# Optimization experiments

Measured on AMD Instinct MI355X. Metric: run time of the kernel, lower is better.

Reference implementation:

```python
import jax, jax.numpy as jnp
import numpy as np

D_MODEL = 1024
NUM_HEADS = 16
HEAD_DIM = D_MODEL // NUM_HEADS
THETA = 10000.0


def _init_linear(key, d_out, d_in):
    sigma = np.sqrt(2.0 / (d_in + d_out))
    w = jax.random.truncated_normal(key, -3.0, 3.0, (d_out, d_in), dtype=jnp.float32)
    return w * sigma


def setup_inputs() -> dict:
    key = jax.random.key(0)
    kh, kq, kk, kv, ko = jax.random.split(key, 5)
    h = jax.random.normal(kh, (2, 2048, D_MODEL), dtype=jnp.float32)
    return {
        "h": h,
        "wq": _init_linear(kq, D_MODEL, D_MODEL),
        "wk": _init_linear(kk, D_MODEL, D_MODEL),
        "wv": _init_linear(kv, D_MODEL, D_MODEL),
        "wo": _init_linear(ko, D_MODEL, D_MODEL),
    }


def _rope(x, pos):
    # x: [B, H, T, dh]; rotate interleaved pairs (..., 2k, 2k+1)
    dh = x.shape[-1]
    freq = THETA ** (-jnp.arange(0, dh // 2, dtype=jnp.float32) / (dh // 2))
    ang = pos[:, None] * freq[None, :]            # [T, dh/2]
    cos, sin = jnp.cos(ang), jnp.sin(ang)
    xr = x.reshape(*x.shape[:-1], dh // 2, 2)
    x0, x1 = xr[..., 0], xr[..., 1]
    out = jnp.stack((cos * x0 - sin * x1, sin * x0 + cos * x1), axis=-1)
    return out.reshape(x.shape)


def reference(h, wq, wk, wv, wo):
    B, T, D = h.shape
    Hn, dh = NUM_HEADS, HEAD_DIM

    def split_heads(x):  # [B,T,D] -> [B,H,T,dh]
        return x.reshape(B, T, Hn, dh).transpose(0, 2, 1, 3)

    Q = split_heads(h @ wq.T)
    K = split_heads(h @ wk.T)
    V = split_heads(h @ wv.T)

    pos = jnp.arange(T, dtype=jnp.float32)
    Q = _rope(Q, pos)
    K = _rope(K, pos)

    scores = jnp.einsum('bhqd,bhkd->bhqk', Q, K) / jnp.sqrt(jnp.float32(dh))
    mask = jnp.tril(jnp.ones((T, T), dtype=bool))
    scores = jnp.where(mask, scores, -jnp.inf)
    attn = jax.nn.softmax(scores, axis=-1)
    out = jnp.einsum('bhqk,bhkd->bhqd', attn, V)   # [B,H,T,dh]
    out = out.transpose(0, 2, 1, 3).reshape(B, T, D)
    return out @ wo.T
```

## Files before the change

kernel.cpp:

```cpp
#include <hip/hip_runtime.h>
#include <math.h>

typedef __bf16 bf16_t;
typedef __bf16 v8bf __attribute__((ext_vector_type(8)));
typedef __bf16 v4bf __attribute__((ext_vector_type(4)));
typedef float  v4f  __attribute__((ext_vector_type(4)));

#define AS1 __attribute__((address_space(1)))
#define AS3 __attribute__((address_space(3)))

static __device__ __forceinline__ void load_lds16(const bf16_t* g, bf16_t* l) {
    __builtin_amdgcn_global_load_lds((AS1 void*)const_cast<bf16_t*>(g),
                                     (AS3 void*)l, 16, 0, 0);
}

__global__ __launch_bounds__(256) void cvt_fp32_bf16(
    const float* __restrict__ h,  const float* __restrict__ wq,
    const float* __restrict__ wk, const float* __restrict__ wv,
    const float* __restrict__ wo,
    bf16_t* __restrict__ hb,  bf16_t* __restrict__ wqb,
    bf16_t* __restrict__ wkb, bf16_t* __restrict__ wvb,
    bf16_t* __restrict__ wob)
{
    const size_t HM = (size_t)4 << 20;
    const size_t i8 = ((size_t)blockIdx.x * 256 + threadIdx.x) * 8;
    const float* src; bf16_t* dst; size_t off;
    if (i8 < HM) { src = h; dst = hb; off = i8; }
    else {
        const size_t r = (i8 - HM) >> 20;
        off = (i8 - HM) & (((size_t)1 << 20) - 1);
        src = (r == 0) ? wq  : (r == 1) ? wk  : (r == 2) ? wv  : wo;
        dst = (r == 0) ? wqb : (r == 1) ? wkb : (r == 2) ? wvb : wob;
    }
    const float4 a = *(const float4*)(src + off);
    const float4 b = *(const float4*)(src + off + 4);
    v8bf o;
    o[0]=(bf16_t)a.x; o[1]=(bf16_t)a.y; o[2]=(bf16_t)a.z; o[3]=(bf16_t)a.w;
    o[4]=(bf16_t)b.x; o[5]=(bf16_t)b.y; o[6]=(bf16_t)b.z; o[7]=(bf16_t)b.w;
    *(v8bf*)(dst + off) = o;
}

static __device__ __forceinline__ void fast_sincos(float ang, float* sn, float* cs) {
    float rv = ang * 0.15915494309189535f;
    rv -= floorf(rv);
    const float a = rv * 6.283185307179586f;
    *sn = __sinf(a);
    *cs = __cosf(a);
}

__global__ __launch_bounds__(256) void qkv_gemm_rope(
    const bf16_t* __restrict__ A,
    const bf16_t* __restrict__ wq,
    const bf16_t* __restrict__ wk,
    const bf16_t* __restrict__ wv,
    bf16_t* __restrict__ qo, bf16_t* __restrict__ ko, bf16_t* __restrict__ vo)
{
    __shared__ __align__(16) bf16_t smem[17408];
    bf16_t* As = smem;
    bf16_t* Bs = smem + 4096;

    const int tid = threadIdx.x;
    const int n0  = blockIdx.x * 128;
    const int m0  = blockIdx.y * 128;
    const int sel = n0 >> 10;
    const bf16_t* W = (sel == 0) ? wq : (sel == 1) ? wk : wv;
    const int wr0 = n0 & 1023;

    const int wave = tid >> 6;
    const int lane = tid & 63;
    const int l16  = lane & 15;
    const int quad = lane >> 4;
    const int wrow = (wave >> 1) * 64;
    const int wcol = (wave & 1) * 64;

    v4f acc[4][4];
    #pragma unroll
    for (int i = 0; i < 4; ++i)
        #pragma unroll
        for (int j = 0; j < 4; ++j) acc[i][j] = (v4f)(0.0f);

    for (int kt = 0; kt < 32; ++kt) {
        const int k0 = kt * 32;
        #pragma unroll
        for (int rep = 0; rep < 2; ++rep) {
            const int c   = rep * 256 + tid;
            const int row = c >> 2;
            const int col = (c & 3) * 8;
            load_lds16(A + (size_t)(m0 + row) * 1024 + k0 + col, &As[c * 8]);
            load_lds16(W + (size_t)(wr0 + row) * 1024 + k0 + col, &Bs[c * 8]);
        }
        __syncthreads();

        v8bf af[4], bfb[4];
        #pragma unroll
        for (int i = 0; i < 4; ++i) {
            af[i]  = *(const v8bf*)&As[(wrow + i * 16 + l16) * 32 + quad * 8];
            bfb[i] = *(const v8bf*)&Bs[(wcol + i * 16 + l16) * 32 + quad * 8];
        }
        #pragma unroll
        for (int i = 0; i < 4; ++i)
            #pragma unroll
            for (int j = 0; j < 4; ++j)
                acc[i][j] = __builtin_amdgcn_mfma_f32_16x16x32_bf16(
                    af[i], bfb[j], acc[i][j], 0, 0, 0);
        __syncthreads();
    }

    bf16_t* Ls = smem + wave * 4352;
    const int bq     = (m0 + wrow) >> 11;
    const int hd     = ((n0 + wcol) >> 6) & 15;
    const int t_base = (m0 + wrow) & 2047;

    if (sel < 2) {
        bf16_t* OUT = (sel == 0) ? qo : ko;
        #pragma unroll
        for (int i = 0; i < 4; ++i) {
            #pragma unroll
            for (int j = 0; j < 4; ++j) {
                #pragma unroll
                for (int r = 0; r < 4; ++r) {
                    const int mrow = i * 16 + quad * 4 + r;
                    const int dcol = j * 16 + l16;
                    float v = acc[i][j][r];
                    const float vp = __shfl_xor(v, 1);
                    const int t  = t_base + mrow;
                    const int kk = dcol >> 1;
                    const float freq = exp2f((float)kk * -0.4152410118609203f);
                    float sn, cs;
                    fast_sincos((float)t * freq, &sn, &cs);
                    v = ((dcol & 1) == 0) ? (cs * v - sn * vp) : (sn * vp + cs * v);
                    Ls[mrow * 68 + dcol] = (bf16_t)v;
                }
            }
        }
        #pragma unroll
        for (int s = 0; s < 8; ++s) {
            const int row = s * 8 + (lane >> 3);
            const int off = (lane & 7) * 8;
            const v8bf vv = *(const v8bf*)&Ls[row * 68 + off];
            *(v8bf*)(OUT + (((size_t)(bq * 16 + hd) * 2048) + t_base + row) * 64 + off) = vv;
        }
    } else {
        #pragma unroll
        for (int i = 0; i < 4; ++i)
            #pragma unroll
            for (int j = 0; j < 4; ++j) {
                v4bf p;
                #pragma unroll
                for (int r = 0; r < 4; ++r) p[r] = (bf16_t)acc[i][j][r];
                *(v4bf*)&Ls[(j * 16 + l16) * 68 + i * 16 + quad * 4] = p;
            }
        #pragma unroll
        for (int s = 0; s < 8; ++s) {
            const int drow = s * 8 + (lane >> 3);
            const int off  = (lane & 7) * 8;
            const v8bf vv = *(const v8bf*)&Ls[drow * 68 + off];
            *(v8bf*)(vo + (((size_t)(bq * 16 + hd) * 64) + drow) * 2048 + t_base + off) = vv;
        }
    }
}

__global__ __launch_bounds__(256) void attn_mfma(
    const bf16_t* __restrict__ qg,
    const bf16_t* __restrict__ kg,
    const bf16_t* __restrict__ vtg,
    bf16_t* __restrict__ og)
{
    __shared__ __align__(16) bf16_t Ks[64 * 72];
    __shared__ __align__(16) bf16_t Vs[64 * 72];
    __shared__ __align__(16) bf16_t Ps[4][16 * 72];

    const int tid  = threadIdx.x;
    const int wave = tid >> 6;
    const int lane = tid & 63;
    const int l16  = lane & 15;
    const int quad = lane >> 4;

    const int i    = blockIdx.x;
    const int pair = (i >> 3) & 15;
    const int bh   = (i & 7) * 4 + (i >> 7);
    const int b = bh >> 4, hh = bh & 15;

    const bf16_t* Kb = kg  + (size_t)bh * 2048 * 64;
    const bf16_t* Vb = vtg + (size_t)bh * 64 * 2048;

    #pragma unroll
    for (int pass = 0; pass < 2; ++pass) {
        const int qt   = pass ? pair : (31 - pair);
        const int qglb = qt * 64 + wave * 16 + l16;

        const bf16_t* qrow = qg + ((size_t)bh * 2048 + qglb) * 64;
        v8bf qf[2];
        qf[0] = *(const v8bf*)(qrow + quad * 8);
        qf[1] = *(const v8bf*)(qrow + 32 + quad * 8);
        #pragma unroll
        for (int e = 0; e < 8; ++e) {
            qf[0][e] = (bf16_t)((float)qf[0][e] * 0.125f);
            qf[1][e] = (bf16_t)((float)qf[1][e] * 0.125f);
        }

        float m_r = -1e30f, l_r = 0.0f;
        v4f o_acc[4];
        #pragma unroll
        for (int d = 0; d < 4; ++d) o_acc[d] = (v4f)(0.0f);

        v8bf kreg[2], vreg[2];
        #pragma unroll
        for (int rep = 0; rep < 2; ++rep) {
            const int c = rep * 256 + tid;
            const int row = c >> 3, col = (c & 7) * 8;
            kreg[rep] = *(const v8bf*)(Kb + (size_t)row * 64 + col);
            vreg[rep] = *(const v8bf*)(Vb + (size_t)row * 2048 + col);
        }

        for (int kt = 0; kt <= qt; ++kt) {
            __syncthreads();
            #pragma unroll
            for (int rep = 0; rep < 2; ++rep) {
                const int c = rep * 256 + tid;
                const int row = c >> 3, col = (c & 7) * 8;
                *(v8bf*)&Ks[row * 72 + col] = kreg[rep];
                *(v8bf*)&Vs[row * 72 + col] = vreg[rep];
            }
            __syncthreads();

            if (kt < qt) {
                #pragma unroll
                for (int rep = 0; rep < 2; ++rep) {
                    const int c = rep * 256 + tid;
                    const int row = c >> 3, col = (c & 7) * 8;
                    kreg[rep] = *(const v8bf*)(Kb + ((size_t)(kt + 1) * 64 + row) * 64 + col);
                    vreg[rep] = *(const v8bf*)(Vb + (size_t)row * 2048 + (kt + 1) * 64 + col);
                }
            }

            v4f s_acc[4];
            #pragma unroll
            for (int kblk = 0; kblk < 4; ++kblk) s_acc[kblk] = (v4f)(0.0f);
            #pragma unroll
            for (int kblk = 0; kblk < 4; ++kblk) {
                const v8bf kf0 = *(const v8bf*)&Ks[(kblk * 16 + l16) * 72 + quad * 8];
                const v8bf kf1 = *(const v8bf*)&Ks[(kblk * 16 + l16) * 72 + 32 + quad * 8];
                s_acc[kblk] = __builtin_amdgcn_mfma_f32_16x16x32_bf16(
                    kf0, qf[0], s_acc[kblk], 0, 0, 0);
                s_acc[kblk] = __builtin_amdgcn_mfma_f32_16x16x32_bf16(
                    kf1, qf[1], s_acc[kblk], 0, 0, 0);
            }

            if (kt == qt) {
                #pragma unroll
                for (int kblk = 0; kblk < 4; ++kblk)
                    #pragma unroll
                    for (int r = 0; r < 4; ++r)
                        if (kblk * 16 + quad * 4 + r > wave * 16 + l16)
                            s_acc[kblk][r] = -1e30f;
            }

            float mx = -1e30f;
            #pragma unroll
            for (int kblk = 0; kblk < 4; ++kblk)
                #pragma unroll
                for (int r = 0; r < 4; ++r) mx = fmaxf(mx, s_acc[kblk][r]);
            mx = fmaxf(mx, __shfl_xor(mx, 16));
            mx = fmaxf(mx, __shfl_xor(mx, 32));
            const float m_new = fmaxf(m_r, mx);
            float ssum = 0.0f;
            #pragma unroll
            for (int kblk = 0; kblk < 4; ++kblk)
                #pragma unroll
                for (int r = 0; r < 4; ++r) {
                    const float p = __expf(s_acc[kblk][r] - m_new);
                    s_acc[kblk][r] = p;
                    ssum += p;
                }
            ssum += __shfl_xor(ssum, 16);
            ssum += __shfl_xor(ssum, 32);
            const float alpha = __expf(m_r - m_new);
            l_r = l_r * alpha + ssum;
            m_r = m_new;

            #pragma unroll
            for (int kblk = 0; kblk < 4; ++kblk) {
                v4bf p;
                #pragma unroll
                for (int r = 0; r < 4; ++r) p[r] = (bf16_t)s_acc[kblk][r];
                *(v4bf*)&Ps[wave][l16 * 72 + kblk * 16 + quad * 4] = p;
            }
            #pragma unroll
            for (int d = 0; d < 4; ++d) o_acc[d] *= alpha;

            const v8bf pf0 = *(const v8bf*)&Ps[wave][l16 * 72 + quad * 8];
            const v8bf pf1 = *(const v8bf*)&Ps[wave][l16 * 72 + 32 + quad * 8];
            #pragma unroll
            for (int dblk = 0; dblk < 4; ++dblk) {
                const v8bf vf0 = *(const v8bf*)&Vs[(dblk * 16 + l16) * 72 + quad * 8];
                const v8bf vf1 = *(const v8bf*)&Vs[(dblk * 16 + l16) * 72 + 32 + quad * 8];
                o_acc[dblk] = __builtin_amdgcn_mfma_f32_16x16x32_bf16(
                    vf0, pf0, o_acc[dblk], 0, 0, 0);
                o_acc[dblk] = __builtin_amdgcn_mfma_f32_16x16x32_bf16(
                    vf1, pf1, o_acc[dblk], 0, 0, 0);
            }
        }

        const float inv_l = 1.0f / l_r;
        const size_t base = ((size_t)b * 2048 + qglb) * 1024 + hh * 64;
        #pragma unroll
        for (int dblk = 0; dblk < 4; ++dblk) {
            v4bf o;
            #pragma unroll
            for (int r = 0; r < 4; ++r) o[r] = (bf16_t)(o_acc[dblk][r] * inv_l);
            *(v4bf*)(og + base + dblk * 16 + quad * 4) = o;
        }
    }
}

__global__ __launch_bounds__(256) void out_gemm(
    const bf16_t* __restrict__ A,
    const bf16_t* __restrict__ W,
    float* __restrict__ C)
{
    __shared__ __align__(16) float smemf[8448];
    bf16_t* As = (bf16_t*)smemf;
    bf16_t* Bs = As + 4096;

    const int tid = threadIdx.x;
    const int n0  = blockIdx.x * 128;
    const int m0  = blockIdx.y * 128;

    const int wave = tid >> 6;
    const int lane = tid & 63;
    const int l16  = lane & 15;
    const int quad = lane >> 4;
    const int wrow = (wave >> 1) * 64;
    const int wcol = (wave & 1) * 64;

    v4f acc[4][4];
    #pragma unroll
    for (int i = 0; i < 4; ++i)
        #pragma unroll
        for (int j = 0; j < 4; ++j) acc[i][j] = (v4f)(0.0f);

    for (int kt = 0; kt < 32; ++kt) {
        const int k0 = kt * 32;
        #pragma unroll
        for (int rep = 0; rep < 2; ++rep) {
            const int c   = rep * 256 + tid;
            const int row = c >> 2;
            const int col = (c & 3) * 8;
            load_lds16(A + (size_t)(m0 + row) * 1024 + k0 + col, &As[c * 8]);
            load_lds16(W + (size_t)(n0 + row) * 1024 + k0 + col, &Bs[c * 8]);
        }
        __syncthreads();

        v8bf af[4], bfb[4];
        #pragma unroll
        for (int i = 0; i < 4; ++i) {
            af[i]  = *(const v8bf*)&As[(wrow + i * 16 + l16) * 32 + quad * 8];
            bfb[i] = *(const v8bf*)&Bs[(wcol + i * 16 + l16) * 32 + quad * 8];
        }
        #pragma unroll
        for (int i = 0; i < 4; ++i)
            #pragma unroll
            for (int j = 0; j < 4; ++j)
                acc[i][j] = __builtin_amdgcn_mfma_f32_16x16x32_bf16(
                    af[i], bfb[j], acc[i][j], 0, 0, 0);
        __syncthreads();
    }

    float* Lw = smemf + wave * 2112;
    #pragma unroll
    for (int half = 0; half < 2; ++half) {
        #pragma unroll
        for (int ii = 0; ii < 2; ++ii) {
            const int i = half * 2 + ii;
            #pragma unroll
            for (int j = 0; j < 4; ++j)
                #pragma unroll
                for (int r = 0; r < 4; ++r)
                    Lw[(ii * 16 + quad * 4 + r) * 66 + j * 16 + l16] = acc[i][j][r];
        }
        __syncthreads();
        #pragma unroll
        for (int s = 0; s < 16; ++s) {
            const int row = s * 2 + (lane >> 5);
            const int off = (lane & 31) * 2;
            const float2 vv = *(const float2*)&Lw[row * 66 + off];
            *(float2*)(C + (size_t)(m0 + wrow + half * 32 + row) * 1024 + n0 + wcol + off) = vv;
        }
        __syncthreads();
    }
}

extern "C" void kernel_launch(void* const* d_in, const int* in_sizes, int n_in,
                              void* d_out, int out_size, void* d_ws, size_t ws_size,
                              hipStream_t stream) {
    const float* h  = (const float*)d_in[0];
    const float* wq = (const float*)d_in[1];
    const float* wk = (const float*)d_in[2];
    const float* wv = (const float*)d_in[3];
    const float* wo = (const float*)d_in[4];

    const size_t NH = (size_t)4096 * 1024;
    const size_t NW = (size_t)1024 * 1024;

    bf16_t* hb  = (bf16_t*)d_ws;
    bf16_t* wqb = hb  + NH;
    bf16_t* wkb = wqb + NW;
    bf16_t* wvb = wkb + NW;
    bf16_t* wvv = wvb;
    bf16_t* wob = wvb + NW;
    bf16_t* qw  = wob + NW;
    bf16_t* kw  = qw + NH;
    bf16_t* vw  = kw + NH;
    bf16_t* og  = hb;
    (void)wvv;

    cvt_fp32_bf16<<<dim3(4096), dim3(256), 0, stream>>>(
        h, wq, wk, wv, wo, hb, wqb, wkb, wvb, wob);
    qkv_gemm_rope<<<dim3(24, 32), dim3(256), 0, stream>>>(hb, wqb, wkb, wvb, qw, kw, vw);
    attn_mfma<<<dim3(512), dim3(256), 0, stream>>>(qw, kw, vw, og);
    out_gemm<<<dim3(8, 32), dim3(256), 0, stream>>>(og, wob, (float*)d_out);
}
```

Measured before the change: 189.6 us.

## Split attention query-tile pairs into separate blocks and precompute RoPE table

```diff
diff --git a/kernel.cpp b/kernel.cpp
--- a/kernel.cpp
+++ b/kernel.cpp
@@ -12,6 +12,14 @@
 static __device__ __forceinline__ void load_lds16(const bf16_t* g, bf16_t* l) {
     __builtin_amdgcn_global_load_lds((AS1 void*)const_cast<bf16_t*>(g),
                                      (AS3 void*)l, 16, 0, 0);
+}
+
+static __device__ __forceinline__ void fast_sincos(float ang, float* sn, float* cs) {
+    float rv = ang * 0.15915494309189535f;
+    rv -= floorf(rv);
+    const float a = rv * 6.283185307179586f;
+    *sn = __sinf(a);
+    *cs = __cosf(a);
 }
 
 __global__ __launch_bounds__(256) void cvt_fp32_bf16(
@@ -20,8 +28,18 @@
     const float* __restrict__ wo,
     bf16_t* __restrict__ hb,  bf16_t* __restrict__ wqb,
     bf16_t* __restrict__ wkb, bf16_t* __restrict__ wvb,
-    bf16_t* __restrict__ wob)
+    bf16_t* __restrict__ wob, float2* __restrict__ rtab)
 {
+    if (blockIdx.x >= 4096) {
+        const int idx = (blockIdx.x - 4096) * 256 + threadIdx.x;
+        const int t  = idx >> 5;
+        const int kk = idx & 31;
+        const float freq = exp2f((float)kk * -0.4152410118609203f);
+        float sn, cs;
+        fast_sincos((float)t * freq, &sn, &cs);
+        rtab[idx] = make_float2(cs, sn);
+        return;
+    }
     const size_t HM = (size_t)4 << 20;
     const size_t i8 = ((size_t)blockIdx.x * 256 + threadIdx.x) * 8;
     const float* src; bf16_t* dst; size_t off;
@@ -40,19 +58,12 @@
     *(v8bf*)(dst + off) = o;
 }
 
-static __device__ __forceinline__ void fast_sincos(float ang, float* sn, float* cs) {
-    float rv = ang * 0.15915494309189535f;
-    rv -= floorf(rv);
-    const float a = rv * 6.283185307179586f;
-    *sn = __sinf(a);
-    *cs = __cosf(a);
-}
-
 __global__ __launch_bounds__(256) void qkv_gemm_rope(
     const bf16_t* __restrict__ A,
     const bf16_t* __restrict__ wq,
     const bf16_t* __restrict__ wk,
     const bf16_t* __restrict__ wv,
+    const float2* __restrict__ rtab,
     bf16_t* __restrict__ qo, bf16_t* __restrict__ ko, bf16_t* __restrict__ vo)
 {
     __shared__ __align__(16) bf16_t smem[17408];
@@ -125,10 +136,9 @@
                     const float vp = __shfl_xor(v, 1);
                     const int t  = t_base + mrow;
                     const int kk = dcol >> 1;
-                    const float freq = exp2f((float)kk * -0.4152410118609203f);
-                    float sn, cs;
-                    fast_sincos((float)t * freq, &sn, &cs);
-                    v = ((dcol & 1) == 0) ? (cs * v - sn * vp) : (sn * vp + cs * v);
+                    const float2 cs = rtab[t * 32 + kk];
+                    v = ((dcol & 1) == 0) ? (cs.x * v - cs.y * vp)
+                                          : (cs.y * vp + cs.x * v);
                     Ls[mrow * 68 + dcol] = (bf16_t)v;
                 }
             }
@@ -176,141 +186,140 @@
     const int l16  = lane & 15;
     const int quad = lane >> 4;
 
-    const int i    = blockIdx.x;
-    const int pair = (i >> 3) & 15;
-    const int bh   = (i & 7) * 4 + (i >> 7);
+    const int i  = blockIdx.x;
+    const int tt = i >> 3;
+    const int u  = tt & 31;
+    const int g  = tt >> 5;
+    const int qt = (g & 1) ? u : (31 - u);
+    const int bh = (i & 7) * 4 + g;
     const int b = bh >> 4, hh = bh & 15;
 
     const bf16_t* Kb = kg  + (size_t)bh * 2048 * 64;
     const bf16_t* Vb = vtg + (size_t)bh * 64 * 2048;
 
-    #pragma unroll
-    for (int pass = 0; pass < 2; ++pass) {
-        const int qt   = pass ? pair : (31 - pair);
-        const int qglb = qt * 64 + wave * 16 + l16;
-
-        const bf16_t* qrow = qg + ((size_t)bh * 2048 + qglb) * 64;
-        v8bf qf[2];
-        qf[0] = *(const v8bf*)(qrow + quad * 8);
-        qf[1] = *(const v8bf*)(qrow + 32 + quad * 8);
-        #pragma unroll
-        for (int e = 0; e < 8; ++e) {
-            qf[0][e] = (bf16_t)((float)qf[0][e] * 0.125f);
-            qf[1][e] = (bf16_t)((float)qf[1][e] * 0.125f);
-        }
-
-        float m_r = -1e30f, l_r = 0.0f;
-        v4f o_acc[4];
-        #pragma unroll
-        for (int d = 0; d < 4; ++d) o_acc[d] = (v4f)(0.0f);
-
-        v8bf kreg[2], vreg[2];
+    const int qglb = qt * 64 + wave * 16 + l16;
+
+    const bf16_t* qrow = qg + ((size_t)bh * 2048 + qglb) * 64;
+    v8bf qf[2];
+    qf[0] = *(const v8bf*)(qrow + quad * 8);
+    qf[1] = *(const v8bf*)(qrow + 32 + quad * 8);
+    #pragma unroll
+    for (int e = 0; e < 8; ++e) {
+        qf[0][e] = (bf16_t)((float)qf[0][e] * 0.125f);
+        qf[1][e] = (bf16_t)((float)qf[1][e] * 0.125f);
+    }
+
+    float m_r = -1e30f, l_r = 0.0f;
+    v4f o_acc[4];
+    #pragma unroll
+    for (int d = 0; d < 4; ++d) o_acc[d] = (v4f)(0.0f);
+
+    v8bf kreg[2], vreg[2];
+    #pragma unroll
+    for (int rep = 0; rep < 2; ++rep) {
+        const int c = rep * 256 + tid;
+        const int row = c >> 3, col = (c & 7) * 8;
+        kreg[rep] = *(const v8bf*)(Kb + (size_t)row * 64 + col);
+        vreg[rep] = *(const v8bf*)(Vb + (size_t)row * 2048 + col);
+    }
+
+    for (int kt = 0; kt <= qt; ++kt) {
+        __syncthreads();
         #pragma unroll
         for (int rep = 0; rep < 2; ++rep) {
             const int c = rep * 256 + tid;
             const int row = c >> 3, col = (c & 7) * 8;
-            kreg[rep] = *(const v8bf*)(Kb + (size_t)row * 64 + col);
-            vreg[rep] = *(const v8bf*)(Vb + (size_t)row * 2048 + col);
-        }
-
-        for (int kt = 0; kt <= qt; ++kt) {
-            __syncthreads();
+            *(v8bf*)&Ks[row * 72 + col] = kreg[rep];
+            *(v8bf*)&Vs[row * 72 + col] = vreg[rep];
+        }
+        __syncthreads();
+
+        if (kt < qt) {
             #pragma unroll
             for (int rep = 0; rep < 2; ++rep) {
                 const int c = rep * 256 + tid;
                 const int row = c >> 3, col = (c & 7) * 8;
-                *(v8bf*)&Ks[row * 72 + col] = kreg[rep];
-                *(v8bf*)&Vs[row * 72 + col] = vreg[rep];
+                kreg[rep] = *(const v8bf*)(Kb + ((size_t)(kt + 1) * 64 + row) * 64 + col);
+                vreg[rep] = *(const v8bf*)(Vb + (size_t)row * 2048 + (kt + 1) * 64 + col);
             }
-            __syncthreads();
-
-            if (kt < qt) {
-                #pragma unroll
-                for (int rep = 0; rep < 2; ++rep) {
-                    const int c = rep * 256 + tid;
-                    const int row = c >> 3, col = (c & 7) * 8;
-                    kreg[rep] = *(const v8bf*)(Kb + ((size_t)(kt + 1) * 64 + row) * 64 + col);
-                    vreg[rep] = *(const v8bf*)(Vb + (size_t)row * 2048 + (kt + 1) * 64 + col);
-                }
-            }
-
-            v4f s_acc[4];
-            #pragma unroll
-            for (int kblk = 0; kblk < 4; ++kblk) s_acc[kblk] = (v4f)(0.0f);
-            #pragma unroll
-            for (int kblk = 0; kblk < 4; ++kblk) {
-                const v8bf kf0 = *(const v8bf*)&Ks[(kblk * 16 + l16) * 72 + quad * 8];
-                const v8bf kf1 = *(const v8bf*)&Ks[(kblk * 16 + l16) * 72 + 32 + quad * 8];
-                s_acc[kblk] = __builtin_amdgcn_mfma_f32_16x16x32_bf16(
-                    kf0, qf[0], s_acc[kblk], 0, 0, 0);
-                s_acc[kblk] = __builtin_amdgcn_mfma_f32_16x16x32_bf16(
-                    kf1, qf[1], s_acc[kblk], 0, 0, 0);
-            }
-
-            if (kt == qt) {
-                #pragma unroll
-                for (int kblk = 0; kblk < 4; ++kblk)
-                    #pragma unroll
-                    for (int r = 0; r < 4; ++r)
-                        if (kblk * 16 + quad * 4 + r > wave * 16 + l16)
-                            s_acc[kblk][r] = -1e30f;
-            }
-
-            float mx = -1e30f;
+        }
+
+        v4f s_acc[4];
+        #pragma unroll
+        for (int kblk = 0; kblk < 4; ++kblk) s_acc[kblk] = (v4f)(0.0f);
+        #pragma unroll
+        for (int kblk = 0; kblk < 4; ++kblk) {
+            const v8bf kf0 = *(const v8bf*)&Ks[(kblk * 16 + l16) * 72 + quad * 8];
+            const v8bf kf1 = *(const v8bf*)&Ks[(kblk * 16 + l16) * 72 + 32 + quad * 8];
+            s_acc[kblk] = __builtin_amdgcn_mfma_f32_16x16x32_bf16(
+                kf0, qf[0], s_acc[kblk], 0, 0, 0);
+            s_acc[kblk] = __builtin_amdgcn_mfma_f32_16x16x32_bf16(
+                kf1, qf[1], s_acc[kblk], 0, 0, 0);
+        }
+
+        if (kt == qt) {
             #pragma unroll
             for (int kblk = 0; kblk < 4; ++kblk)
                 #pragma unroll
-                for (int r = 0; r < 4; ++r) mx = fmaxf(mx, s_acc[kblk][r]);
-            mx = fmaxf(mx, __shfl_xor(mx, 16));
-            mx = fmaxf(mx, __shfl_xor(mx, 32));
-            const float m_new = fmaxf(m_r, mx);
-            float ssum = 0.0f;
-            #pragma unroll
-            for (int kblk = 0; kblk < 4; ++kblk)
-                #pragma unroll
-                for (int r = 0; r < 4; ++r) {
-                    const float p = __expf(s_acc[kblk][r] - m_new);
-                    s_acc[kblk][r] = p;
-                    ssum += p;
-                }
-            ssum += __shfl_xor(ssum, 16);
-            ssum += __shfl_xor(ssum, 32);
-            const float alpha = __expf(m_r - m_new);
-            l_r = l_r * alpha + ssum;
-            m_r = m_new;
-
-            #pragma unroll
-            for (int kblk = 0; kblk < 4; ++kblk) {
-                v4bf p;
-                #pragma unroll
-                for (int r = 0; r < 4; ++r) p[r] = (bf16_t)s_acc[kblk][r];
-                *(v4bf*)&Ps[wave][l16 * 72 + kblk * 16 + quad * 4] = p;
+                for (int r = 0; r < 4; ++r)
+                    if (kblk * 16 + quad * 4 + r > wave * 16 + l16)
+                        s_acc[kblk][r] = -1e30f;
+        }
+
+        float mx = -1e30f;
+        #pragma unroll
+        for (int kblk = 0; kblk < 4; ++kblk)
+            #pragma unroll
+            for (int r = 0; r < 4; ++r) mx = fmaxf(mx, s_acc[kblk][r]);
+        mx = fmaxf(mx, __shfl_xor(mx, 16));
+        mx = fmaxf(mx, __shfl_xor(mx, 32));
+        const float m_new = fmaxf(m_r, mx);
+        float ssum = 0.0f;
+        #pragma unroll
+        for (int kblk = 0; kblk < 4; ++kblk)
+            #pragma unroll
+            for (int r = 0; r < 4; ++r) {
+                const float p = __expf(s_acc[kblk][r] - m_new);
+                s_acc[kblk][r] = p;
+                ssum += p;
             }
-            #pragma unroll
-            for (int d = 0; d < 4; ++d) o_acc[d] *= alpha;
-
-            const v8bf pf0 = *(const v8bf*)&Ps[wave][l16 * 72 + quad * 8];
-            const v8bf pf1 = *(const v8bf*)&Ps[wave][l16 * 72 + 32 + quad * 8];
-            #pragma unroll
-            for (int dblk = 0; dblk < 4; ++dblk) {
-                const v8bf vf0 = *(const v8bf*)&Vs[(dblk * 16 + l16) * 72 + quad * 8];
-                const v8bf vf1 = *(const v8bf*)&Vs[(dblk * 16 + l16) * 72 + 32 + quad * 8];
-                o_acc[dblk] = __builtin_amdgcn_mfma_f32_16x16x32_bf16(
-                    vf0, pf0, o_acc[dblk], 0, 0, 0);
-                o_acc[dblk] = __builtin_amdgcn_mfma_f32_16x16x32_bf16(
-                    vf1, pf1, o_acc[dblk], 0, 0, 0);
-            }
-        }
-
-        const float inv_l = 1.0f / l_r;
-        const size_t base = ((size_t)b * 2048 + qglb) * 1024 + hh * 64;
+        ssum += __shfl_xor(ssum, 16);
+        ssum += __shfl_xor(ssum, 32);
+        const float alpha = __expf(m_r - m_new);
+        l_r = l_r * alpha + ssum;
+        m_r = m_new;
+
+        #pragma unroll
+        for (int kblk = 0; kblk < 4; ++kblk) {
+            v4bf p;
+            #pragma unroll
+            for (int r = 0; r < 4; ++r) p[r] = (bf16_t)s_acc[kblk][r];
+            *(v4bf*)&Ps[wave][l16 * 72 + kblk * 16 + quad * 4] = p;
+        }
+        #pragma unroll
+        for (int d = 0; d < 4; ++d) o_acc[d] *= alpha;
+
+        const v8bf pf0 = *(const v8bf*)&Ps[wave][l16 * 72 + quad * 8];
+        const v8bf pf1 = *(const v8bf*)&Ps[wave][l16 * 72 + 32 + quad * 8];
         #pragma unroll
         for (int dblk = 0; dblk < 4; ++dblk) {
-            v4bf o;
-            #pragma unroll
-            for (int r = 0; r < 4; ++r) o[r] = (bf16_t)(o_acc[dblk][r] * inv_l);
-            *(v4bf*)(og + base + dblk * 16 + quad * 4) = o;
-        }
+            const v8bf vf0 = *(const v8bf*)&Vs[(dblk * 16 + l16) * 72 + quad * 8];
+            const v8bf vf1 = *(const v8bf*)&Vs[(dblk * 16 + l16) * 72 + 32 + quad * 8];
+            o_acc[dblk] = __builtin_amdgcn_mfma_f32_16x16x32_bf16(
+                vf0, pf0, o_acc[dblk], 0, 0, 0);
+            o_acc[dblk] = __builtin_amdgcn_mfma_f32_16x16x32_bf16(
+                vf1, pf1, o_acc[dblk], 0, 0, 0);
+        }
+    }
+
+    const float inv_l = 1.0f / l_r;
+    const size_t base = ((size_t)b * 2048 + qglb) * 1024 + hh * 64;
+    #pragma unroll
+    for (int dblk = 0; dblk < 4; ++dblk) {
+        v4bf o;
+        #pragma unroll
+        for (int r = 0; r < 4; ++r) o[r] = (bf16_t)(o_acc[dblk][r] * inv_l);
+        *(v4bf*)(og + base + dblk * 16 + quad * 4) = o;
     }
 }
 
@@ -407,17 +416,17 @@
     bf16_t* wqb = hb  + NH;
     bf16_t* wkb = wqb + NW;
     bf16_t* wvb = wkb + NW;
-    bf16_t* wvv = wvb;
     bf16_t* wob = wvb + NW;
     bf16_t* qw  = wob + NW;
     bf16_t* kw  = qw + NH;
     bf16_t* vw  = kw + NH;
+    float2* rtab = (float2*)(vw + NH);
     bf16_t* og  = hb;
-    (void)wvv;
-
-    cvt_fp32_bf16<<<dim3(4096), dim3(256), 0, stream>>>(
-        h, wq, wk, wv, wo, hb, wqb, wkb, wvb, wob);
-    qkv_gemm_rope<<<dim3(24, 32), dim3(256), 0, stream>>>(hb, wqb, wkb, wvb, qw, kw, vw);
-    attn_mfma<<<dim3(512), dim3(256), 0, stream>>>(qw, kw, vw, og);
+
+    cvt_fp32_bf16<<<dim3(4352), dim3(256), 0, stream>>>(
+        h, wq, wk, wv, wo, hb, wqb, wkb, wvb, wob, rtab);
+    qkv_gemm_rope<<<dim3(24, 32), dim3(256), 0, stream>>>(
+        hb, wqb, wkb, wvb, rtab, qw, kw, vw);
+    attn_mfma<<<dim3(1024), dim3(256), 0, stream>>>(qw, kw, vw, og);
     out_gemm<<<dim3(8, 32), dim3(256), 0, stream>>>(og, wob, (float*)d_out);
 }
```

After: 214.0 us. 1.13x slower.

## Split attention into one q-tile per block, read V fragments from global, use exp2

Applied to the files above, without the earlier changes.

```diff
diff --git a/kernel.cpp b/kernel.cpp
--- a/kernel.cpp
+++ b/kernel.cpp
@@ -12,6 +12,14 @@
 static __device__ __forceinline__ void load_lds16(const bf16_t* g, bf16_t* l) {
     __builtin_amdgcn_global_load_lds((AS1 void*)const_cast<bf16_t*>(g),
                                      (AS3 void*)l, 16, 0, 0);
+}
+
+static __device__ __forceinline__ void fast_sincos(float ang, float* sn, float* cs) {
+    float rv = ang * 0.15915494309189535f;
+    rv -= floorf(rv);
+    const float a = rv * 6.283185307179586f;
+    *sn = __sinf(a);
+    *cs = __cosf(a);
 }
 
 __global__ __launch_bounds__(256) void cvt_fp32_bf16(
@@ -40,14 +48,6 @@
     *(v8bf*)(dst + off) = o;
 }
 
-static __device__ __forceinline__ void fast_sincos(float ang, float* sn, float* cs) {
-    float rv = ang * 0.15915494309189535f;
-    rv -= floorf(rv);
-    const float a = rv * 6.283185307179586f;
-    *sn = __sinf(a);
-    *cs = __cosf(a);
-}
-
 __global__ __launch_bounds__(256) void qkv_gemm_rope(
     const bf16_t* __restrict__ A,
     const bf16_t* __restrict__ wq,
@@ -160,14 +160,13 @@
     }
 }
 
-__global__ __launch_bounds__(256) void attn_mfma(
+__global__ __launch_bounds__(256, 4) void attn_mfma(
     const bf16_t* __restrict__ qg,
     const bf16_t* __restrict__ kg,
     const bf16_t* __restrict__ vtg,
     bf16_t* __restrict__ og)
 {
     __shared__ __align__(16) bf16_t Ks[64 * 72];
-    __shared__ __align__(16) bf16_t Vs[64 * 72];
     __shared__ __align__(16) bf16_t Ps[4][16 * 72];
 
     const int tid  = threadIdx.x;
@@ -176,141 +175,143 @@
     const int l16  = lane & 15;
     const int quad = lane >> 4;
 
-    const int i    = blockIdx.x;
-    const int pair = (i >> 3) & 15;
-    const int bh   = (i & 7) * 4 + (i >> 7);
+    const int i  = blockIdx.x;
+    const int tt = i >> 3;
+    const int u  = tt & 31;
+    const int g  = tt >> 5;
+    const int qt = (g & 1) ? u : (31 - u);
+    const int bh = (i & 7) * 4 + g;
     const int b = bh >> 4, hh = bh & 15;
 
     const bf16_t* Kb = kg  + (size_t)bh * 2048 * 64;
     const bf16_t* Vb = vtg + (size_t)bh * 64 * 2048;
 
-    #pragma unroll
-    for (int pass = 0; pass < 2; ++pass) {
-        const int qt   = pass ? pair : (31 - pair);
-        const int qglb = qt * 64 + wave * 16 + l16;
-
-        const bf16_t* qrow = qg + ((size_t)bh * 2048 + qglb) * 64;
-        v8bf qf[2];
-        qf[0] = *(const v8bf*)(qrow + quad * 8);
-        qf[1] = *(const v8bf*)(qrow + 32 + quad * 8);
-        #pragma unroll
-        for (int e = 0; e < 8; ++e) {
-            qf[0][e] = (bf16_t)((float)qf[0][e] * 0.125f);
-            qf[1][e] = (bf16_t)((float)qf[1][e] * 0.125f);
-        }
-
-        float m_r = -1e30f, l_r = 0.0f;
-        v4f o_acc[4];
-        #pragma unroll
-        for (int d = 0; d < 4; ++d) o_acc[d] = (v4f)(0.0f);
-
-        v8bf kreg[2], vreg[2];
+    const int qglb = qt * 64 + wave * 16 + l16;
+
+    const bf16_t* qrow = qg + ((size_t)bh * 2048 + qglb) * 64;
+    v8bf qf[2];
+    qf[0] = *(const v8bf*)(qrow + quad * 8);
+    qf[1] = *(const v8bf*)(qrow + 32 + quad * 8);
+    #pragma unroll
+    for (int e = 0; e < 8; ++e) {
+        qf[0][e] = (bf16_t)((float)qf[0][e] * 0.18033688011112042f);
+        qf[1][e] = (bf16_t)((float)qf[1][e] * 0.18033688011112042f);
+    }
+
+    float m_r = -1e30f, l_r = 0.0f;
+    v4f o_acc[4];
+    #pragma unroll
+    for (int d = 0; d < 4; ++d) o_acc[d] = (v4f)(0.0f);
+
+    v8bf kreg[2];
+    #pragma unroll
+    for (int rep = 0; rep < 2; ++rep) {
+        const int c = rep * 256 + tid;
+        const int row = c >> 3, col = (c & 7) * 8;
+        kreg[rep] = *(const v8bf*)(Kb + (size_t)row * 64 + col);
+    }
+
+    for (int kt = 0; kt <= qt; ++kt) {
+        __syncthreads();
         #pragma unroll
         for (int rep = 0; rep < 2; ++rep) {
             const int c = rep * 256 + tid;
             const int row = c >> 3, col = (c & 7) * 8;
-            kreg[rep] = *(const v8bf*)(Kb + (size_t)row * 64 + col);
-            vreg[rep] = *(const v8bf*)(Vb + (size_t)row * 2048 + col);
-        }
-
-        for (int kt = 0; kt <= qt; ++kt) {
-            __syncthreads();
+            *(v8bf*)&Ks[row * 72 + col] = kreg[rep];
+        }
+        __syncthreads();
+
+        if (kt < qt) {
             #pragma unroll
             for (int rep = 0; rep < 2; ++rep) {
                 const int c = rep * 256 + tid;
                 const int row = c >> 3, col = (c & 7) * 8;
-                *(v8bf*)&Ks[row * 72 + col] = kreg[rep];
-                *(v8bf*)&Vs[row * 72 + col] = vreg[rep];
+                kreg[rep] = *(const v8bf*)(Kb + ((size_t)(kt + 1) * 64 + row) * 64 + col);
             }
-            __syncthreads();
-
-            if (kt < qt) {
-                #pragma unroll
-                for (int rep = 0; rep < 2; ++rep) {
-                    const int c = rep * 256 + tid;
-                    const int row = c >> 3, col = (c & 7) * 8;
-                    kreg[rep] = *(const v8bf*)(Kb + ((size_t)(kt + 1) * 64 + row) * 64 + col);
-                    vreg[rep] = *(const v8bf*)(Vb + (size_t)row * 2048 + (kt + 1) * 64 + col);
-                }
-            }
-
-            v4f s_acc[4];
-            #pragma unroll
-            for (int kblk = 0; kblk < 4; ++kblk) s_acc[kblk] = (v4f)(0.0f);
-            #pragma unroll
-            for (int kblk = 0; kblk < 4; ++kblk) {
-                const v8bf kf0 = *(const v8bf*)&Ks[(kblk * 16 + l16) * 72 + quad * 8];
-                const v8bf kf1 = *(const v8bf*)&Ks[(kblk * 16 + l16) * 72 + 32 + quad * 8];
-                s_acc[kblk] = __builtin_amdgcn_mfma_f32_16x16x32_bf16(
-                    kf0, qf[0], s_acc[kblk], 0, 0, 0);
-                s_acc[kblk] = __builtin_amdgcn_mfma_f32_16x16x32_bf16(
-                    kf1, qf[1], s_acc[kblk], 0, 0, 0);
-            }
-
-            if (kt == qt) {
-                #pragma unroll
-                for (int kblk = 0; kblk < 4; ++kblk)
-                    #pragma unroll
-                    for (int r = 0; r < 4; ++r)
-                        if (kblk * 16 + quad * 4 + r > wave * 16 + l16)
-                            s_acc[kblk][r] = -1e30f;
-            }
-
-            float mx = -1e30f;
+        }
+
+        v8bf vf[4][2];
+        #pragma unroll
+        for (int dblk = 0; dblk < 4; ++dblk) {
+            const bf16_t* vrow = Vb + (size_t)(dblk * 16 + l16) * 2048 + kt * 64;
+            vf[dblk][0] = *(const v8bf*)(vrow + quad * 8);
+            vf[dblk][1] = *(const v8bf*)(vrow + 32 + quad * 8);
+        }
+
+        v4f s_acc[4];
+        #pragma unroll
+        for (int kblk = 0; kblk < 4; ++kblk) s_acc[kblk] = (v4f)(0.0f);
+        #pragma unroll
+        for (int kblk = 0; kblk < 4; ++kblk) {
+            const v8bf kf0 = *(const v8bf*)&Ks[(kblk * 16 + l16) * 72 + quad * 8];
+            const v8bf kf1 = *(const v8bf*)&Ks[(kblk * 16 + l16) * 72 + 32 + quad * 8];
+            s_acc[kblk] = __builtin_amdgcn_mfma_f32_16x16x32_bf16(
+                kf0, qf[0], s_acc[kblk], 0, 0, 0);
+            s_acc[kblk] = __builtin_amdgcn_mfma_f32_16x16x32_bf16(
+                kf1, qf[1], s_acc[kblk], 0, 0, 0);
+        }
+
+        if (kt == qt) {
             #pragma unroll
             for (int kblk = 0; kblk < 4; ++kblk)
                 #pragma unroll
-                for (int r = 0; r < 4; ++r) mx = fmaxf(mx, s_acc[kblk][r]);
-            mx = fmaxf(mx, __shfl_xor(mx, 16));
-            mx = fmaxf(mx, __shfl_xor(mx, 32));
-            const float m_new = fmaxf(m_r, mx);
-            float ssum = 0.0f;
-            #pragma unroll
-            for (int kblk = 0; kblk < 4; ++kblk)
-                #pragma unroll
-                for (int r = 0; r < 4; ++r) {
-                    const float p = __expf(s_acc[kblk][r] - m_new);
-                    s_acc[kblk][r] = p;
-                    ssum += p;
-                }
-            ssum += __shfl_xor(ssum, 16);
-            ssum += __shfl_xor(ssum, 32);
-            const float alpha = __expf(m_r - m_new);
-            l_r = l_r * alpha + ssum;
-            m_r = m_new;
-
-            #pragma unroll
-            for (int kblk = 0; kblk < 4; ++kblk) {
-                v4bf p;
-                #pragma unroll
-                for (int r = 0; r < 4; ++r) p[r] = (bf16_t)s_acc[kblk][r];
-                *(v4bf*)&Ps[wave][l16 * 72 + kblk * 16 + quad * 4] = p;
+                for (int r = 0; r < 4; ++r)
+                    if (kblk * 16 + quad * 4 + r > wave * 16 + l16)
+                        s_acc[kblk][r] = -1e30f;
+        }
+
+        float mx = -1e30f;
+        #pragma unroll
+        for (int kblk = 0; kblk < 4; ++kblk)
+            #pragma unroll
+            for (int r = 0; r < 4; ++r) mx = fmaxf(mx, s_acc[kblk][r]);
+        mx = fmaxf(mx, __shfl_xor(mx, 16));
+        mx = fmaxf(mx, __shfl_xor(mx, 32));
+        const float m_new = fmaxf(m_r, mx);
+        float ssum = 0.0f;
+        #pragma unroll
+        for (int kblk = 0; kblk < 4; ++kblk)
+            #pragma unroll
+            for (int r = 0; r < 4; ++r) {
+                const float p = exp2f(s_acc[kblk][r] - m_new);
+                s_acc[kblk][r] = p;
+                ssum += p;
             }
-            #pragma unroll
-            for (int d = 0; d < 4; ++d) o_acc[d] *= alpha;
-
-            const v8bf pf0 = *(const v8bf*)&Ps[wave][l16 * 72 + quad * 8];
-            const v8bf pf1 = *(const v8bf*)&Ps[wave][l16 * 72 + 32 + quad * 8];
-            #pragma unroll
-            for (int dblk = 0; dblk < 4; ++dblk) {
-                const v8bf vf0 = *(const v8bf*)&Vs[(dblk * 16 + l16) * 72 + quad * 8];
-                const v8bf vf1 = *(const v8bf*)&Vs[(dblk * 16 + l16) * 72 + 32 + quad * 8];
-                o_acc[dblk] = __builtin_amdgcn_mfma_f32_16x16x32_bf16(
-                    vf0, pf0, o_acc[dblk], 0, 0, 0);
-                o_acc[dblk] = __builtin_amdgcn_mfma_f32_16x16x32_bf16(
-                    vf1, pf1, o_acc[dblk], 0, 0, 0);
-            }
-        }
-
-        const float inv_l = 1.0f / l_r;
-        const size_t base = ((size_t)b * 2048 + qglb) * 1024 + hh * 64;
+        ssum += __shfl_xor(ssum, 16);
+        ssum += __shfl_xor(ssum, 32);
+        const float alpha = exp2f(m_r - m_new);
+        l_r = l_r * alpha + ssum;
+        m_r = m_new;
+
+        #pragma unroll
+        for (int kblk = 0; kblk < 4; ++kblk) {
+            v4bf p;
+            #pragma unroll
+            for (int r = 0; r < 4; ++r) p[r] = (bf16_t)s_acc[kblk][r];
+            *(v4bf*)&Ps[wave][l16 * 72 + kblk * 16 + quad * 4] = p;
+        }
+        #pragma unroll
+        for (int d = 0; d < 4; ++d) o_acc[d] *= alpha;
+
+        const v8bf pf0 = *(const v8bf*)&Ps[wave][l16 * 72 + quad * 8];
+        const v8bf pf1 = *(const v8bf*)&Ps[wave][l16 * 72 + 32 + quad * 8];
         #pragma unroll
         for (int dblk = 0; dblk < 4; ++dblk) {
-            v4bf o;
-            #pragma unroll
-            for (int r = 0; r < 4; ++r) o[r] = (bf16_t)(o_acc[dblk][r] * inv_l);
-            *(v4bf*)(og + base + dblk * 16 + quad * 4) = o;
-        }
+            o_acc[dblk] = __builtin_amdgcn_mfma_f32_16x16x32_bf16(
+                vf[dblk][0], pf0, o_acc[dblk], 0, 0, 0);
+            o_acc[dblk] = __builtin_amdgcn_mfma_f32_16x16x32_bf16(
+                vf[dblk][1], pf1, o_acc[dblk], 0, 0, 0);
+        }
+    }
+
+    const float inv_l = 1.0f / l_r;
+    const size_t base = ((size_t)b * 2048 + qglb) * 1024 + hh * 64;
+    #pragma unroll
+    for (int dblk = 0; dblk < 4; ++dblk) {
+        v4bf o;
+        #pragma unroll
+        for (int r = 0; r < 4; ++r) o[r] = (bf16_t)(o_acc[dblk][r] * inv_l);
+        *(v4bf*)(og + base + dblk * 16 + quad * 4) = o;
     }
 }
 
@@ -407,17 +408,16 @@
     bf16_t* wqb = hb  + NH;
     bf16_t* wkb = wqb + NW;
     bf16_t* wvb = wkb + NW;
-    bf16_t* wvv = wvb;
     bf16_t* wob = wvb + NW;
     bf16_t* qw  = wob + NW;
     bf16_t* kw  = qw + NH;
     bf16_t* vw  = kw + NH;
     bf16_t* og  = hb;
-    (void)wvv;
 
     cvt_fp32_bf16<<<dim3(4096), dim3(256), 0, stream>>>(
         h, wq, wk, wv, wo, hb, wqb, wkb, wvb, wob);
-    qkv_gemm_rope<<<dim3(24, 32), dim3(256), 0, stream>>>(hb, wqb, wkb, wvb, qw, kw, vw);
-    attn_mfma<<<dim3(512), dim3(256), 0, stream>>>(qw, kw, vw, og);
+    qkv_gemm_rope<<<dim3(24, 32), dim3(256), 0, stream>>>(
+        hb, wqb, wkb, wvb, qw, kw, vw);
+    attn_mfma<<<dim3(1024), dim3(256), 0, stream>>>(qw, kw, vw, og);
     out_gemm<<<dim3(8, 32), dim3(256), 0, stream>>>(og, wob, (float*)d_out);
 }
```

Measured after the change: 214.3 us. +13.1%, slower.

## Process 128 query rows per attention block so each K/V tile serves two groups

Applied to the files above, without the earlier changes.

```diff
diff --git a/kernel.cpp b/kernel.cpp
--- a/kernel.cpp
+++ b/kernel.cpp
@@ -12,6 +12,14 @@
 static __device__ __forceinline__ void load_lds16(const bf16_t* g, bf16_t* l) {
     __builtin_amdgcn_global_load_lds((AS1 void*)const_cast<bf16_t*>(g),
                                      (AS3 void*)l, 16, 0, 0);
+}
+
+static __device__ __forceinline__ void fast_sincos(float ang, float* sn, float* cs) {
+    float rv = ang * 0.15915494309189535f;
+    rv -= floorf(rv);
+    const float a = rv * 6.283185307179586f;
+    *sn = __sinf(a);
+    *cs = __cosf(a);
 }
 
 __global__ __launch_bounds__(256) void cvt_fp32_bf16(
@@ -40,14 +48,6 @@
     *(v8bf*)(dst + off) = o;
 }
 
-static __device__ __forceinline__ void fast_sincos(float ang, float* sn, float* cs) {
-    float rv = ang * 0.15915494309189535f;
-    rv -= floorf(rv);
-    const float a = rv * 6.283185307179586f;
-    *sn = __sinf(a);
-    *cs = __cosf(a);
-}
-
 __global__ __launch_bounds__(256) void qkv_gemm_rope(
     const bf16_t* __restrict__ A,
     const bf16_t* __restrict__ wq,
@@ -168,7 +168,7 @@
 {
     __shared__ __align__(16) bf16_t Ks[64 * 72];
     __shared__ __align__(16) bf16_t Vs[64 * 72];
-    __shared__ __align__(16) bf16_t Ps[4][16 * 72];
+    __shared__ __align__(16) bf16_t Ps[4][32 * 72];
 
     const int tid  = threadIdx.x;
     const int wave = tid >> 6;
@@ -176,139 +176,168 @@
     const int l16  = lane & 15;
     const int quad = lane >> 4;
 
-    const int i    = blockIdx.x;
-    const int pair = (i >> 3) & 15;
-    const int bh   = (i & 7) * 4 + (i >> 7);
+    const int i  = blockIdx.x;
+    const int tt = i >> 3;
+    const int u  = tt & 15;
+    const int g  = tt >> 4;
+    const int q128 = (((g + 1) >> 1) & 1) ? (15 - u) : u;
+    const int bh = (i & 7) * 4 + g;
     const int b = bh >> 4, hh = bh & 15;
 
     const bf16_t* Kb = kg  + (size_t)bh * 2048 * 64;
     const bf16_t* Vb = vtg + (size_t)bh * 64 * 2048;
 
-    #pragma unroll
-    for (int pass = 0; pass < 2; ++pass) {
-        const int qt   = pass ? pair : (31 - pair);
-        const int qglb = qt * 64 + wave * 16 + l16;
-
-        const bf16_t* qrow = qg + ((size_t)bh * 2048 + qglb) * 64;
-        v8bf qf[2];
-        qf[0] = *(const v8bf*)(qrow + quad * 8);
-        qf[1] = *(const v8bf*)(qrow + 32 + quad * 8);
+    int qglb[2];
+    qglb[0] = q128 * 128 + wave * 16 + l16;
+    qglb[1] = qglb[0] + 64;
+
+    v8bf qf[2][2];
+    #pragma unroll
+    for (int mg = 0; mg < 2; ++mg) {
+        const bf16_t* qrow = qg + ((size_t)bh * 2048 + qglb[mg]) * 64;
+        qf[mg][0] = *(const v8bf*)(qrow + quad * 8);
+        qf[mg][1] = *(const v8bf*)(qrow + 32 + quad * 8);
         #pragma unroll
         for (int e = 0; e < 8; ++e) {
-            qf[0][e] = (bf16_t)((float)qf[0][e] * 0.125f);
-            qf[1][e] = (bf16_t)((float)qf[1][e] * 0.125f);
-        }
-
-        float m_r = -1e30f, l_r = 0.0f;
-        v4f o_acc[4];
-        #pragma unroll
-        for (int d = 0; d < 4; ++d) o_acc[d] = (v4f)(0.0f);
-
-        v8bf kreg[2], vreg[2];
+            qf[mg][0][e] = (bf16_t)((float)qf[mg][0][e] * 0.18033688011112042f);
+            qf[mg][1][e] = (bf16_t)((float)qf[mg][1][e] * 0.18033688011112042f);
+        }
+    }
+
+    float m_r[2] = {-1e30f, -1e30f}, l_r[2] = {0.0f, 0.0f};
+    v4f o_acc[2][4];
+    #pragma unroll
+    for (int mg = 0; mg < 2; ++mg)
+        #pragma unroll
+        for (int d = 0; d < 4; ++d) o_acc[mg][d] = (v4f)(0.0f);
+
+    const int ktmax = 2 * q128 + 1;
+
+    v8bf kreg[2], vreg[2];
+    #pragma unroll
+    for (int rep = 0; rep < 2; ++rep) {
+        const int c = rep * 256 + tid;
+        const int row = c >> 3, col = (c & 7) * 8;
+        kreg[rep] = *(const v8bf*)(Kb + (size_t)row * 64 + col);
+        vreg[rep] = *(const v8bf*)(Vb + (size_t)row * 2048 + col);
+    }
+
+    for (int kt = 0; kt <= ktmax; ++kt) {
+        __syncthreads();
         #pragma unroll
         for (int rep = 0; rep < 2; ++rep) {
             const int c = rep * 256 + tid;
             const int row = c >> 3, col = (c & 7) * 8;
-            kreg[rep] = *(const v8bf*)(Kb + (size_t)row * 64 + col);
-            vreg[rep] = *(const v8bf*)(Vb + (size_t)row * 2048 + col);
-        }
-
-        for (int kt = 0; kt <= qt; ++kt) {
-            __syncthreads();
+            *(v8bf*)&Ks[row * 72 + col] = kreg[rep];
+            *(v8bf*)&Vs[row * 72 + col] = vreg[rep];
+        }
+        __syncthreads();
+
+        if (kt < ktmax) {
             #pragma unroll
             for (int rep = 0; rep < 2; ++rep) {
                 const int c = rep * 256 + tid;
                 const int row = c >> 3, col = (c & 7) * 8;
-                *(v8bf*)&Ks[row * 72 + col] = kreg[rep];
-                *(v8bf*)&Vs[row * 72 + col] = vreg[rep];
-            }
-            __syncthreads();
-
-            if (kt < qt) {
-                #pragma unroll
-                for (int rep = 0; rep < 2; ++rep) {
-                    const int c = rep * 256 + tid;
-                    const int row = c >> 3, col = (c & 7) * 8;
-                    kreg[rep] = *(const v8bf*)(Kb + ((size_t)(kt + 1) * 64 + row) * 64 + col);
-                    vreg[rep] = *(const v8bf*)(Vb + (size_t)row * 2048 + (kt + 1) * 64 + col);
-                }
-            }
-
-            v4f s_acc[4];
-            #pragma unroll
-            for (int kblk = 0; kblk < 4; ++kblk) s_acc[kblk] = (v4f)(0.0f);
-            #pragma unroll
-            for (int kblk = 0; kblk < 4; ++kblk) {
-                const v8bf kf0 = *(const v8bf*)&Ks[(kblk * 16 + l16) * 72 + quad * 8];
-                const v8bf kf1 = *(const v8bf*)&Ks[(kblk * 16 + l16) * 72 + 32 + quad * 8];
-                s_acc[kblk] = __builtin_amdgcn_mfma_f32_16x16x32_bf16(
-                    kf0, qf[0], s_acc[kblk], 0, 0, 0);
-                s_acc[kblk] = __builtin_amdgcn_mfma_f32_16x16x32_bf16(
-                    kf1, qf[1], s_acc[kblk], 0, 0, 0);
-            }
-
-            if (kt == qt) {
+                kreg[rep] = *(const v8bf*)(Kb + ((size_t)(kt + 1) * 64 + row) * 64 + col);
+                vreg[rep] = *(const v8bf*)(Vb + (size_t)row * 2048 + (kt + 1) * 64 + col);
+            }
+        }
+
+        v4f s_acc[2][4];
+        #pragma unroll
+        for (int mg = 0; mg < 2; ++mg)
+            #pragma unroll
+            for (int kblk = 0; kblk < 4; ++kblk) s_acc[mg][kblk] = (v4f)(0.0f);
+        #pragma unroll
+        for (int kblk = 0; kblk < 4; ++kblk) {
+            const v8bf kf0 = *(const v8bf*)&Ks[(kblk * 16 + l16) * 72 + quad * 8];
+            const v8bf kf1 = *(const v8bf*)&Ks[(kblk * 16 + l16) * 72 + 32 + quad * 8];
+            #pragma unroll
+            for (int mg = 0; mg < 2; ++mg) {
+                s_acc[mg][kblk] = __builtin_amdgcn_mfma_f32_16x16x32_bf16(
+                    kf0, qf[mg][0], s_acc[mg][kblk], 0, 0, 0);
+                s_acc[mg][kblk] = __builtin_amdgcn_mfma_f32_16x16x32_bf16(
+                    kf1, qf[mg][1], s_acc[mg][kblk], 0, 0, 0);
+            }
+        }
+
+        #pragma unroll
+        for (int mg = 0; mg < 2; ++mg) {
+            if (kt >= 2 * q128 + mg) {
                 #pragma unroll
                 for (int kblk = 0; kblk < 4; ++kblk)
                     #pragma unroll
                     for (int r = 0; r < 4; ++r)
-                        if (kblk * 16 + quad * 4 + r > wave * 16 + l16)
-                            s_acc[kblk][r] = -1e30f;
-            }
-
+                        if (kt * 64 + kblk * 16 + quad * 4 + r > qglb[mg])
+                            s_acc[mg][kblk][r] = -1e30f;
+            }
+        }
+
+        #pragma unroll
+        for (int mg = 0; mg < 2; ++mg) {
             float mx = -1e30f;
             #pragma unroll
             for (int kblk = 0; kblk < 4; ++kblk)
                 #pragma unroll
-                for (int r = 0; r < 4; ++r) mx = fmaxf(mx, s_acc[kblk][r]);
+                for (int r = 0; r < 4; ++r) mx = fmaxf(mx, s_acc[mg][kblk][r]);
             mx = fmaxf(mx, __shfl_xor(mx, 16));
             mx = fmaxf(mx, __shfl_xor(mx, 32));
-            const float m_new = fmaxf(m_r, mx);
+            const float m_new = fmaxf(m_r[mg], mx);
             float ssum = 0.0f;
             #pragma unroll
             for (int kblk = 0; kblk < 4; ++kblk)
                 #pragma unroll
                 for (int r = 0; r < 4; ++r) {
-                    const float p = __expf(s_acc[kblk][r] - m_new);
-                    s_acc[kblk][r] = p;
+                    const float p = exp2f(s_acc[mg][kblk][r] - m_new);
+                    s_acc[mg][kblk][r] = p;
                     ssum += p;
                 }
             ssum += __shfl_xor(ssum, 16);
             ssum += __shfl_xor(ssum, 32);
-            const float alpha = __expf(m_r - m_new);
-            l_r = l_r * alpha + ssum;
-            m_r = m_new;
+            const float alpha = exp2f(m_r[mg] - m_new);
+            l_r[mg] = l_r[mg] * alpha + ssum;
+            m_r[mg] = m_new;
 
             #pragma unroll
             for (int kblk = 0; kblk < 4; ++kblk) {
                 v4bf p;
                 #pragma unroll
-                for (int r = 0; r < 4; ++r) p[r] = (bf16_t)s_acc[kblk][r];
-                *(v4bf*)&Ps[wave][l16 * 72 + kblk * 16 + quad * 4] = p;
-            }
-            #pragma unroll
-            for (int d = 0; d < 4; ++d) o_acc[d] *= alpha;
-
-            const v8bf pf0 = *(const v8bf*)&Ps[wave][l16 * 72 + quad * 8];
-            const v8bf pf1 = *(const v8bf*)&Ps[wave][l16 * 72 + 32 + quad * 8];
-            #pragma unroll
-            for (int dblk = 0; dblk < 4; ++dblk) {
-                const v8bf vf0 = *(const v8bf*)&Vs[(dblk * 16 + l16) * 72 + quad * 8];
-                const v8bf vf1 = *(const v8bf*)&Vs[(dblk * 16 + l16) * 72 + 32 + quad * 8];
-                o_acc[dblk] = __builtin_amdgcn_mfma_f32_16x16x32_bf16(
-                    vf0, pf0, o_acc[dblk], 0, 0, 0);
-                o_acc[dblk] = __builtin_amdgcn_mfma_f32_16x16x32_bf16(
-                    vf1, pf1, o_acc[dblk], 0, 0, 0);
-            }
-        }
-
-        const float inv_l = 1.0f / l_r;
-        const size_t base = ((size_t)b * 2048 + qglb) * 1024 + hh * 64;
+                for (int r = 0; r < 4; ++r) p[r] = (bf16_t)s_acc[mg][kblk][r];
+                *(v4bf*)&Ps[wave][(mg * 16 + l16) * 72 + kblk * 16 + quad * 4] = p;
+            }
+            #pragma unroll
+            for (int d = 0; d < 4; ++d) o_acc[mg][d] *= alpha;
+        }
+
+        v8bf pf[2][2];
+        #pragma unroll
+        for (int mg = 0; mg < 2; ++mg) {
+            pf[mg][0] = *(const v8bf*)&Ps[wave][(mg * 16 + l16) * 72 + quad * 8];
+            pf[mg][1] = *(const v8bf*)&Ps[wave][(mg * 16 + l16) * 72 + 32 + quad * 8];
+        }
+        #pragma unroll
+        for (int dblk = 0; dblk < 4; ++dblk) {
+            const v8bf vf0 = *(const v8bf*)&Vs[(dblk * 16 + l16) * 72 + quad * 8];
+            const v8bf vf1 = *(const v8bf*)&Vs[(dblk * 16 + l16) * 72 + 32 + quad * 8];
+            #pragma unroll
+            for (int mg = 0; mg < 2; ++mg) {
+                o_acc[mg][dblk] = __builtin_amdgcn_mfma_f32_16x16x32_bf16(
+                    vf0, pf[mg][0], o_acc[mg][dblk], 0, 0, 0);
+                o_acc[mg][dblk] = __builtin_amdgcn_mfma_f32_16x16x32_bf16(
+                    vf1, pf[mg][1], o_acc[mg][dblk], 0, 0, 0);
+            }
+        }
+    }
+
+    #pragma unroll
+    for (int mg = 0; mg < 2; ++mg) {
+        const float inv_l = 1.0f / l_r[mg];
+        const size_t base = ((size_t)b * 2048 + qglb[mg]) * 1024 + hh * 64;
         #pragma unroll
         for (int dblk = 0; dblk < 4; ++dblk) {
             v4bf o;
             #pragma unroll
-            for (int r = 0; r < 4; ++r) o[r] = (bf16_t)(o_acc[dblk][r] * inv_l);
+            for (int r = 0; r < 4; ++r) o[r] = (bf16_t)(o_acc[mg][dblk][r] * inv_l);
             *(v4bf*)(og + base + dblk * 16 + quad * 4) = o;
         }
     }
@@ -407,17 +436,16 @@
     bf16_t* wqb = hb  + NH;
     bf16_t* wkb = wqb + NW;
     bf16_t* wvb = wkb + NW;
-    bf16_t* wvv = wvb;
     bf16_t* wob = wvb + NW;
     bf16_t* qw  = wob + NW;
     bf16_t* kw  = qw + NH;
     bf16_t* vw  = kw + NH;
     bf16_t* og  = hb;
-    (void)wvv;
 
     cvt_fp32_bf16<<<dim3(4096), dim3(256), 0, stream>>>(
         h, wq, wk, wv, wo, hb, wqb, wkb, wvb, wob);
-    qkv_gemm_rope<<<dim3(24, 32), dim3(256), 0, stream>>>(hb, wqb, wkb, wvb, qw, kw, vw);
+    qkv_gemm_rope<<<dim3(24, 32), dim3(256), 0, stream>>>(
+        hb, wqb, wkb, wvb, qw, kw, vw);
     attn_mfma<<<dim3(512), dim3(256), 0, stream>>>(qw, kw, vw, og);
     out_gemm<<<dim3(8, 32), dim3(256), 0, stream>>>(og, wob, (float*)d_out);
 }
```

After: 203.4 us. +7.3%, slower.
